# Optimization experiments

Measured on AMD Instinct MI355X. Metric: run time of the kernel, lower is better.

## Reference

```python
import jax, jax.numpy as jnp
import numpy as np

USER_NUM = 100000
ITEM_NUM = 50000
EMBED = 64
N_LAYERS = 3
E_RATE = 2000000
E_TRUST = 500000
E_PRED = 100000


def setup_inputs() -> dict:
    key = jax.random.key(0)
    ks = jax.random.split(key, 10)
    return {
        "emb_user": jax.random.normal(ks[0], (USER_NUM, EMBED), dtype=jnp.float32),
        "emb_item": jax.random.normal(ks[1], (ITEM_NUM, EMBED), dtype=jnp.float32),
        "rate_u": jax.random.randint(ks[2], (E_RATE,), 0, USER_NUM, dtype=jnp.int32),
        "rate_i": jax.random.randint(ks[3], (E_RATE,), 0, ITEM_NUM, dtype=jnp.int32),
        "trust_src": jax.random.randint(ks[4], (E_TRUST,), 0, USER_NUM, dtype=jnp.int32),
        "trust_dst": jax.random.randint(ks[5], (E_TRUST,), 0, USER_NUM, dtype=jnp.int32),
        "pos_u": jax.random.randint(ks[6], (E_PRED,), 0, USER_NUM, dtype=jnp.int32),
        "pos_i": jax.random.randint(ks[7], (E_PRED,), 0, ITEM_NUM, dtype=jnp.int32),
        "neg_u": jax.random.randint(ks[8], (E_PRED,), 0, USER_NUM, dtype=jnp.int32),
        "neg_i": jax.random.randint(ks[9], (E_PRED,), 0, ITEM_NUM, dtype=jnp.int32),
    }


def _degrees(idx, n):
    # float degree counts, clamped to >=1 (DGL GraphConv clamps zero degrees)
    d = jax.ops.segment_sum(jnp.ones_like(idx, dtype=jnp.float32), idx, num_segments=n)
    return jnp.maximum(d, 1.0)


def _gcn_conv(h_src, src, dst, n_dst, deg_src, deg_dst):
    # GraphConv(norm='both', weight=False, bias=False):
    # out[v] = deg(v)^-1/2 * sum_{u->v} deg(u)^-1/2 * h[u]
    ns = jax.lax.rsqrt(deg_src)
    nd = jax.lax.rsqrt(deg_dst)
    msg = (h_src * ns[:, None])[src]          # [E, D] gather
    agg = jax.ops.segment_sum(msg, dst, num_segments=n_dst)
    return agg * nd[:, None]


def reference(emb_user, emb_item, rate_u, rate_i, trust_src, trust_dst,
              pos_u, pos_i, neg_u, neg_i):
    nU, nI = emb_user.shape[0], emb_item.shape[0]
    deg_u = _degrees(rate_u, nU)       # user degree in rate graph (out for rate, in for rated-by)
    deg_i = _degrees(rate_i, nI)       # item degree in rate graph
    deg_ts = _degrees(trust_src, nU)
    deg_td = _degrees(trust_dst, nU)

    res_u, res_i = emb_user, emb_item
    cur_u, cur_i = emb_user, emb_item
    for _ in range(N_LAYERS):
        # item -> user ('rated-by'): src deg = deg_i, dst deg = deg_u
        new_u = _gcn_conv(cur_i, rate_i, rate_u, nU, deg_i, deg_u)
        # user -> item ('rate')
        new_i = _gcn_conv(cur_u, rate_u, rate_i, nI, deg_u, deg_i)
        # user -> user ('trust'), added into user output
        new_u = new_u + _gcn_conv(cur_u, trust_src, trust_dst, nU, deg_ts, deg_td)
        res_u = res_u + new_u
        res_i = res_i + new_i
        cur_u, cur_i = new_u, new_i

    scale = 1.0 / (N_LAYERS + 1)
    res_u = res_u * scale
    res_i = res_i * scale

    # HeteroDotProductPredictor on 'rate' etype: u_dot_v -> [E, 1]
    pos_score = jnp.sum(res_u[pos_u] * res_i[pos_i], axis=-1, keepdims=True)
    neg_score = jnp.sum(res_u[neg_u] * res_i[neg_i], axis=-1, keepdims=True)
    return pos_score, neg_score
```

## Files before the change

kernel.cpp:

```cpp
#include <hip/hip_runtime.h>
#include <hip/hip_fp16.h>

#define NU 100000
#define NI 50000
#define D  64
#define CAPU 64
#define CAPI 96
#define CAPT 32
#define BS 256

#define NB1 256
#define KPB1 391
#define CAPB1 9216
#define NB2 256
#define KPB2 196
#define CAPB2 9216
#define NB3 128
#define KPB3 782
#define CAPB3 4864
#define NB4 128
#define CAPB4 4864
#define GR 224
#define GT 32

typedef unsigned long long u64;

__global__ void __launch_bounds__(1024) k_binAll(
    const int* __restrict__ ru, const int* __restrict__ ri,
    const int* __restrict__ ts, const int* __restrict__ td,
    int* __restrict__ bc1, int* __restrict__ bc2,
    int* __restrict__ bc3, int* __restrict__ bc4,
    u64* __restrict__ bins1, u64* __restrict__ bins2,
    u64* __restrict__ bins3, u64* __restrict__ bins4,
    int E_rate, int E_trust)
{
    __shared__ int cnt[512];
    __shared__ int base[512];
    int b = blockIdx.x, tid = threadIdx.x;
    if (b < GR) {
        if (tid < 512) cnt[tid] = 0;
        __syncthreads();
        for (int c0 = b * 1024; c0 < E_rate; c0 += GR * 1024) {
            int e = c0 + tid;
            if (e < E_rate) {
                int u = ru[e], it = ri[e];
                atomicAdd(&cnt[u / KPB1], 1);
                atomicAdd(&cnt[256 + it / KPB2], 1);
            }
        }
        __syncthreads();
        if (tid < 256)      base[tid] = atomicAdd(&bc1[tid], cnt[tid]);
        else if (tid < 512) base[tid] = atomicAdd(&bc2[tid - 256], cnt[tid]);
        __syncthreads();
        if (tid < 512) cnt[tid] = 0;
        __syncthreads();
        for (int c0 = b * 1024; c0 < E_rate; c0 += GR * 1024) {
            int e = c0 + tid;
            if (e < E_rate) {
                int u = ru[e], it = ri[e];
                int b1 = u / KPB1, b2 = it / KPB2;
                int r1 = atomicAdd(&cnt[b1], 1);
                int o1 = base[b1] + r1;
                if (o1 < CAPB1) bins1[(size_t)b1 * CAPB1 + o1] = ((u64)u << 32) | (unsigned)it;
                int r2 = atomicAdd(&cnt[256 + b2], 1);
                int o2 = base[256 + b2] + r2;
                if (o2 < CAPB2) bins2[(size_t)b2 * CAPB2 + o2] = ((u64)it << 32) | (unsigned)u;
            }
        }
    } else {
        int bb = b - GR;
        if (tid < 256) cnt[tid] = 0;
        __syncthreads();
        for (int c0 = bb * 1024; c0 < E_trust; c0 += GT * 1024) {
            int e = c0 + tid;
            if (e < E_trust) {
                int s = ts[e], dd = td[e];
                atomicAdd(&cnt[dd / KPB3], 1);
                atomicAdd(&cnt[128 + s / KPB3], 1);
            }
        }
        __syncthreads();
        if (tid < 128)      base[tid] = atomicAdd(&bc3[tid], cnt[tid]);
        else if (tid < 256) base[tid] = atomicAdd(&bc4[tid - 128], cnt[tid]);
        __syncthreads();
        if (tid < 256) cnt[tid] = 0;
        __syncthreads();
        for (int c0 = bb * 1024; c0 < E_trust; c0 += GT * 1024) {
            int e = c0 + tid;
            if (e < E_trust) {
                int s = ts[e], dd = td[e];
                int b3 = dd / KPB3, b4 = s / KPB3;
                int r3 = atomicAdd(&cnt[b3], 1);
                int o3 = base[b3] + r3;
                if (o3 < CAPB3) bins3[(size_t)b3 * CAPB3 + o3] = ((u64)dd << 32) | (unsigned)s;
                int r4 = atomicAdd(&cnt[128 + b4], 1);
                int o4 = base[128 + b4] + r4;
                if (o4 < CAPB4) bins4[(size_t)b4 * CAPB4 + o4] = ((u64)s << 32);
            }
        }
    }
}

__global__ void __launch_bounds__(512) k_buildAll(
    const u64* __restrict__ bins1, const u64* __restrict__ bins2,
    const u64* __restrict__ bins3, const u64* __restrict__ bins4,
    const int* __restrict__ bc1, const int* __restrict__ bc2,
    const int* __restrict__ bc3, const int* __restrict__ bc4,
    int* __restrict__ colU, int* __restrict__ colI, int* __restrict__ colT,
    int* __restrict__ degU, int* __restrict__ degI,
    int* __restrict__ degT, int* __restrict__ degS)
{
    __shared__ int cnt[KPB3];
    int b = blockIdx.x, tid = threadIdx.x;
    const u64* bins; int n, k0, kpb, colcap, nmax; int* col; int* deg;
    if (b < NB1) {
        bins = bins1 + (size_t)b * CAPB1; n = bc1[b]; if (n > CAPB1) n = CAPB1;
        k0 = b * KPB1; kpb = KPB1; colcap = CAPU; col = colU; deg = degU; nmax = NU;
    } else if (b < NB1 + NB2) {
        int q = b - NB1;
        bins = bins2 + (size_t)q * CAPB2; n = bc2[q]; if (n > CAPB2) n = CAPB2;
        k0 = q * KPB2; kpb = KPB2; colcap = CAPI; col = colI; deg = degI; nmax = NI;
    } else if (b < NB1 + NB2 + NB3) {
        int q = b - NB1 - NB2;
        bins = bins3 + (size_t)q * CAPB3; n = bc3[q]; if (n > CAPB3) n = CAPB3;
        k0 = q * KPB3; kpb = KPB3; colcap = CAPT; col = colT; deg = degT; nmax = NU;
    } else {
        int q = b - NB1 - NB2 - NB3;
        bins = bins4 + (size_t)q * CAPB4; n = bc4[q]; if (n > CAPB4) n = CAPB4;
        k0 = q * KPB3; kpb = KPB3; colcap = 0; col = nullptr; deg = degS; nmax = NU;
    }
    for (int t = tid; t < kpb; t += 512) cnt[t] = 0;
    __syncthreads();
    if (col) {
        for (int i = tid; i < n; i += 512) {
            u64 e = bins[i];
            int k = (int)(e >> 32);
            int v = (int)(e & 0xffffffffu);
            int c = atomicAdd(&cnt[k - k0], 1);
            if (c < colcap) col[(size_t)k * colcap + c] = v;
        }
    } else {
        for (int i = tid; i < n; i += 512) {
            int k = (int)(bins[i] >> 32);
            atomicAdd(&cnt[k - k0], 1);
        }
    }
    __syncthreads();
    for (int t = tid; t < kpb; t += 512) {
        int k = k0 + t;
        if (k < nmax) {
            int c = cnt[t];
            if (colcap && c > colcap) c = colcap;
            deg[k] = c;
        }
    }
}

__global__ void k_degrs(const int* __restrict__ degU, const int* __restrict__ degI,
                        const int* __restrict__ degT, const int* __restrict__ degS,
                        float* __restrict__ rs_u, float* __restrict__ rs_i,
                        float* __restrict__ rs_td, float* __restrict__ rs_ts) {
    int i = blockIdx.x * blockDim.x + threadIdx.x;
    if (i < NU) {
        int a = degU[i]; rs_u[i]  = rsqrtf((float)(a < 1 ? 1 : a));
        int b = degT[i]; rs_td[i] = rsqrtf((float)(b < 1 ? 1 : b));
        int c = degS[i]; rs_ts[i] = rsqrtf((float)(c < 1 ? 1 : c));
    }
    if (i < NI) {
        int a = degI[i]; rs_i[i] = rsqrtf((float)(a < 1 ? 1 : a));
    }
}

__global__ void k_inith(const float* __restrict__ src, uint2* __restrict__ cur,
                        uint2* __restrict__ res, int n4) {
    int i = blockIdx.x * blockDim.x + threadIdx.x;
    if (i >= n4) return;
    float4 v = ((const float4*)src)[i];
    uint2 u;
    u.x = ((unsigned)__half_as_ushort(__float2half(v.y)) << 16) |
           (unsigned)__half_as_ushort(__float2half(v.x));
    u.y = ((unsigned)__half_as_ushort(__float2half(v.w)) << 16) |
           (unsigned)__half_as_ushort(__float2half(v.z));
    cur[i] = u;
    res[i] = u;
}


__device__ __forceinline__ void gather32(const int* __restrict__ col, int b, int d,
                                         const float* __restrict__ rs,
                                         const __half2* __restrict__ rows, int gl,
                                         float2& acc) {
    int e = b + d;
    for (int k0 = b; k0 < e; k0 += 32) {
        int idx = k0 + gl;
        int   n = idx < e ? col[idx] : 0;
        float r = idx < e ? rs[n] : 0.f;
        #pragma unroll
        for (int j = 0; j < 32; ++j) {
            int   nn = __shfl(n, j, 32);
            float rr = __shfl(r, j, 32);
            float2 f = __half22float2(rows[(size_t)nn * 32 + gl]);
            acc.x += rr * f.x;
            acc.y += rr * f.y;
        }
    }
}

__device__ __forceinline__ void gather8(const int* __restrict__ col, int b, int d,
                                        const float* __restrict__ rs,
                                        const __half2* __restrict__ rows, int gl,
                                        float2& acc) {
    int e = b + d;
    int sub = gl & 7;
    for (int k0 = b; k0 < e; k0 += 8) {
        int idx = k0 + sub;
        int   n = idx < e ? col[idx] : 0;
        float r = idx < e ? rs[n] : 0.f;
        #pragma unroll
        for (int j = 0; j < 8; ++j) {
            int   nn = __shfl(n, j, 32);
            float rr = __shfl(r, j, 32);
            float2 f = __half22float2(rows[(size_t)nn * 32 + gl]);
            acc.x += rr * f.x;
            acc.y += rr * f.y;
        }
    }
}

__global__ void k_layer(const int* __restrict__ colU, const int* __restrict__ degU,
                        const int* __restrict__ colT, const int* __restrict__ degT,
                        const int* __restrict__ colI, const int* __restrict__ degI,
                        const float* __restrict__ rs_u, const float* __restrict__ rs_i,
                        const float* __restrict__ rs_ts, const float* __restrict__ rs_td,
                        const __half2* __restrict__ cu, const __half2* __restrict__ ci,
                        __half2* __restrict__ nu, __half2* __restrict__ ni,
                        __half2* __restrict__ resu, __half2* __restrict__ resi) {
    int b = blockIdx.x;
    int m = b % 3;
    int base = b / 3;
    int wid = threadIdx.x >> 6;
    int lane = threadIdx.x & 63;
    int grp = lane >> 5;
    int gl  = lane & 31;
    if (m < 2) {
        int node = ((base * 2 + m) * 4 + wid) * 2 + grp;
        if (node >= NU) return;
        float2 acc = {0.f, 0.f}, acc2 = {0.f, 0.f};
        gather32(colU, node * CAPU, degU[node], rs_i, ci, gl, acc);
        gather8 (colT, node * CAPT, degT[node], rs_ts, cu, gl, acc2);
        float su = rs_u[node], st = rs_td[node];
        float vx = su * acc.x + st * acc2.x;
        float vy = su * acc.y + st * acc2.y;
        size_t o = (size_t)node * 32 + gl;
        nu[o] = __floats2half2_rn(vx, vy);
        float2 old = __half22float2(resu[o]);
        resu[o] = __floats2half2_rn(old.x + vx, old.y + vy);
    } else {
        int node = (base * 4 + wid) * 2 + grp;
        if (node >= NI) return;
        float2 acc = {0.f, 0.f};
        gather32(colI, node * CAPI, degI[node], rs_u, cu, gl, acc);
        float si = rs_i[node];
        float vx = si * acc.x, vy = si * acc.y;
        size_t o = (size_t)node * 32 + gl;
        ni[o] = __floats2half2_rn(vx, vy);
        float2 old = __half22float2(resi[o]);
        resi[o] = __floats2half2_rn(old.x + vx, old.y + vy);
    }
}


__global__ void k_pred(const int* __restrict__ pu, const int* __restrict__ pi,
                       const int* __restrict__ nuv, const int* __restrict__ niv,
                       const __half2* __restrict__ ru, const __half2* __restrict__ ri,
                       float* __restrict__ out, int E) {
    long long tid = (long long)blockIdx.x * blockDim.x + threadIdx.x;
    int e = (int)(tid >> 4);
    int c2 = ((int)tid & 15) * 2;
    if (e >= 2 * E) return;
    int ee = (e < E) ? e : e - E;
    int u  = (e < E) ? pu[ee] : nuv[ee];
    int it = (e < E) ? pi[ee] : niv[ee];
    float2 a0 = __half22float2(ru[(size_t)u  * 32 + c2]);
    float2 a1 = __half22float2(ru[(size_t)u  * 32 + c2 + 1]);
    float2 b0 = __half22float2(ri[(size_t)it * 32 + c2]);
    float2 b1 = __half22float2(ri[(size_t)it * 32 + c2 + 1]);
    float s = a0.x * b0.x + a0.y * b0.y + a1.x * b1.x + a1.y * b1.y;
    s += __shfl_xor(s, 1); s += __shfl_xor(s, 2);
    s += __shfl_xor(s, 4); s += __shfl_xor(s, 8);
    if (((int)tid & 15) == 0) out[e] = s * (1.0f / 16.0f);
}

extern "C" void kernel_launch(void* const* d_in, const int* in_sizes, int n_in,
                              void* d_out, int out_size, void* d_ws, size_t ws_size,
                              hipStream_t stream) {
    const float* emb_u  = (const float*)d_in[0];
    const float* emb_i  = (const float*)d_in[1];
    const int* rate_u   = (const int*)d_in[2];
    const int* rate_i   = (const int*)d_in[3];
    const int* trust_s  = (const int*)d_in[4];
    const int* trust_d  = (const int*)d_in[5];
    const int* pos_u    = (const int*)d_in[6];
    const int* pos_i    = (const int*)d_in[7];
    const int* neg_u    = (const int*)d_in[8];
    const int* neg_i    = (const int*)d_in[9];
    const int E_rate  = in_sizes[2];
    const int E_trust = in_sizes[4];
    const int E_pred  = in_sizes[6];

    int* iw   = (int*)d_ws;
    int* degU = iw;
    int* degI = degU + NU;
    int* degT = degI + NI;
    int* degS = degT + NU;
    int* bc1  = degS + NU;
    int* bc2  = bc1 + NB1;
    int* bc3  = bc2 + NB2;
    int* bc4  = bc3 + NB3;
    int* colU = bc4 + NB4;
    int* colI = colU + (size_t)NU * CAPU;
    int* colT = colI + (size_t)NI * CAPI;
    float* rs_u  = (float*)(colT + (size_t)NU * CAPT);
    float* rs_i  = rs_u  + NU;
    float* rs_ts = rs_i  + NI;
    float* rs_td = rs_ts + NU;
    __half2* uA   = (__half2*)(rs_td + NU);
    __half2* uB   = uA + (size_t)NU * 32;
    __half2* iA   = uB + (size_t)NU * 32;
    __half2* iB   = iA + (size_t)NI * 32;
    __half2* res_u = iB + (size_t)NI * 32;
    __half2* res_i = res_u + (size_t)NU * 32;
    u64* bins1 = (u64*)uA;
    u64* bins2 = bins1 + (size_t)NB1 * CAPB1;
    u64* bins3 = bins2 + (size_t)NB2 * CAPB2;
    u64* bins4 = bins3 + (size_t)NB3 * CAPB3;

    hipMemsetAsync(bc1, 0, (NB1 + NB2 + NB3 + NB4) * sizeof(int), stream);

    k_binAll<<<GR + GT, 1024, 0, stream>>>(rate_u, rate_i, trust_s, trust_d,
                                           bc1, bc2, bc3, bc4,
                                           bins1, bins2, bins3, bins4,
                                           E_rate, E_trust);
    k_buildAll<<<NB1 + NB2 + NB3 + NB4, 512, 0, stream>>>(
        bins1, bins2, bins3, bins4, bc1, bc2, bc3, bc4,
        colU, colI, colT, degU, degI, degT, degS);

    k_degrs<<<(NU + BS - 1) / BS, BS, 0, stream>>>(degU, degI, degT, degS,
                                                   rs_u, rs_i, rs_td, rs_ts);

    k_inith<<<(NU * D / 4 + BS - 1) / BS, BS, 0, stream>>>(emb_u, (uint2*)uA, (uint2*)res_u, NU * D / 4);
    k_inith<<<(NI * D / 4 + BS - 1) / BS, BS, 0, stream>>>(emb_i, (uint2*)iA, (uint2*)res_i, NI * D / 4);

    __half2* cu = uA; __half2* nu_ = uB;
    __half2* ci = iA; __half2* ni_ = iB;
    for (int l = 0; l < 3; ++l) {
        k_layer<<<18750, BS, 0, stream>>>(colU, degU, colT, degT, colI, degI,
                                          rs_u, rs_i, rs_ts, rs_td,
                                          cu, ci, nu_, ni_, res_u, res_i);
        __half2* t;
        t = cu; cu = nu_; nu_ = t;
        t = ci; ci = ni_; ni_ = t;
    }

    long long tp = (long long)2 * E_pred * 16;
    k_pred<<<(unsigned)((tp + BS - 1) / BS), BS, 0, stream>>>(
        pos_u, pos_i, neg_u, neg_i, res_u, res_i, (float*)d_out, E_pred);
}
```

Before: 404.3 us.

## Partition neighbor lists by source-index range and split layer into user/item kernels

Adjacency lists are split by neighbor-index range: each node's list is filled from both ends, in two halves for users and trust and four quarters for items. Each segment is then gathered separately, so neighbors of similar index are processed together, aiming for better cache locality on the embedding gathers. The fused layer kernel is also split into separate user and item kernels, which adds a launch per layer and a dependency between them. Degrees are packed as per-class counts and summed in k_degrs, and the extra gather calls add loop overhead for partially filled segments.

```diff
diff --git a/kernel.cpp b/kernel.cpp
--- a/kernel.cpp
+++ b/kernel.cpp
@@ -110,48 +110,106 @@
     int* __restrict__ degU, int* __restrict__ degI,
     int* __restrict__ degT, int* __restrict__ degS)
 {
-    __shared__ int cnt[KPB3];
+    __shared__ int cnt[1568];
     int b = blockIdx.x, tid = threadIdx.x;
-    const u64* bins; int n, k0, kpb, colcap, nmax; int* col; int* deg;
     if (b < NB1) {
-        bins = bins1 + (size_t)b * CAPB1; n = bc1[b]; if (n > CAPB1) n = CAPB1;
-        k0 = b * KPB1; kpb = KPB1; colcap = CAPU; col = colU; deg = degU; nmax = NU;
+        const u64* bins = bins1 + (size_t)b * CAPB1;
+        int n = bc1[b]; if (n > CAPB1) n = CAPB1;
+        int k0 = b * KPB1;
+        for (int t = tid; t < 2 * KPB1; t += 512) cnt[t] = 0;
+        __syncthreads();
+        for (int i = tid; i < n; i += 512) {
+            u64 e = bins[i];
+            int k = (int)(e >> 32) - k0;
+            int v = (int)(e & 0xffffffffu);
+            int cls = v >= (NI / 2);
+            int c = atomicAdd(&cnt[k + cls * KPB1], 1);
+            if (c < CAPU) {
+                int slot = cls ? (CAPU - 1 - c) : c;
+                colU[(size_t)(k0 + k) * CAPU + slot] = v;
+            }
+        }
+        __syncthreads();
+        for (int t = tid; t < KPB1; t += 512) {
+            int k = k0 + t;
+            if (k < NU) {
+                int c0 = cnt[t];          if (c0 > CAPU) c0 = CAPU;
+                int c1 = cnt[t + KPB1];   if (c1 > CAPU) c1 = CAPU;
+                degU[k] = c0 | (c1 << 16);
+            }
+        }
     } else if (b < NB1 + NB2) {
         int q = b - NB1;
-        bins = bins2 + (size_t)q * CAPB2; n = bc2[q]; if (n > CAPB2) n = CAPB2;
-        k0 = q * KPB2; kpb = KPB2; colcap = CAPI; col = colI; deg = degI; nmax = NI;
+        const u64* bins = bins2 + (size_t)q * CAPB2;
+        int n = bc2[q]; if (n > CAPB2) n = CAPB2;
+        int k0 = q * KPB2;
+        for (int t = tid; t < 4 * KPB2; t += 512) cnt[t] = 0;
+        __syncthreads();
+        for (int i = tid; i < n; i += 512) {
+            u64 e = bins[i];
+            int k = (int)(e >> 32) - k0;
+            int v = (int)(e & 0xffffffffu);
+            int cls = v / (NU / 4);
+            int c = atomicAdd(&cnt[k + cls * KPB2], 1);
+            if (c < 48) {
+                int slot = (cls == 0) ? c : (cls == 1) ? (47 - c)
+                         : (cls == 2) ? (48 + c) : (95 - c);
+                colI[(size_t)(k0 + k) * CAPI + slot] = v;
+            }
+        }
+        __syncthreads();
+        for (int t = tid; t < KPB2; t += 512) {
+            int k = k0 + t;
+            if (k < NI) {
+                int c0 = cnt[t];            if (c0 > 48) c0 = 48;
+                int c1 = cnt[t + KPB2];     if (c1 > 48) c1 = 48;
+                int c2 = cnt[t + 2 * KPB2]; if (c2 > 48) c2 = 48;
+                int c3 = cnt[t + 3 * KPB2]; if (c3 > 48) c3 = 48;
+                degI[k] = c0 | (c1 << 8) | (c2 << 16) | (c3 << 24);
+            }
+        }
     } else if (b < NB1 + NB2 + NB3) {
         int q = b - NB1 - NB2;
-        bins = bins3 + (size_t)q * CAPB3; n = bc3[q]; if (n > CAPB3) n = CAPB3;
-        k0 = q * KPB3; kpb = KPB3; colcap = CAPT; col = colT; deg = degT; nmax = NU;
+        const u64* bins = bins3 + (size_t)q * CAPB3;
+        int n = bc3[q]; if (n > CAPB3) n = CAPB3;
+        int k0 = q * KPB3;
+        for (int t = tid; t < 2 * KPB3; t += 512) cnt[t] = 0;
+        __syncthreads();
+        for (int i = tid; i < n; i += 512) {
+            u64 e = bins[i];
+            int k = (int)(e >> 32) - k0;
+            int v = (int)(e & 0xffffffffu);
+            int cls = v >= (NU / 2);
+            int c = atomicAdd(&cnt[k + cls * KPB3], 1);
+            if (c < CAPT) {
+                int slot = cls ? (CAPT - 1 - c) : c;
+                colT[(size_t)(k0 + k) * CAPT + slot] = v;
+            }
+        }
+        __syncthreads();
+        for (int t = tid; t < KPB3; t += 512) {
+            int k = k0 + t;
+            if (k < NU) {
+                int c0 = cnt[t];          if (c0 > CAPT) c0 = CAPT;
+                int c1 = cnt[t + KPB3];   if (c1 > CAPT) c1 = CAPT;
+                degT[k] = c0 | (c1 << 16);
+            }
+        }
     } else {
         int q = b - NB1 - NB2 - NB3;
-        bins = bins4 + (size_t)q * CAPB4; n = bc4[q]; if (n > CAPB4) n = CAPB4;
-        k0 = q * KPB3; kpb = KPB3; colcap = 0; col = nullptr; deg = degS; nmax = NU;
-    }
-    for (int t = tid; t < kpb; t += 512) cnt[t] = 0;
-    __syncthreads();
-    if (col) {
-        for (int i = tid; i < n; i += 512) {
-            u64 e = bins[i];
-            int k = (int)(e >> 32);
-            int v = (int)(e & 0xffffffffu);
-            int c = atomicAdd(&cnt[k - k0], 1);
-            if (c < colcap) col[(size_t)k * colcap + c] = v;
-        }
-    } else {
+        const u64* bins = bins4 + (size_t)q * CAPB4;
+        int n = bc4[q]; if (n > CAPB4) n = CAPB4;
+        int k0 = q * KPB3;
+        for (int t = tid; t < KPB3; t += 512) cnt[t] = 0;
+        __syncthreads();
         for (int i = tid; i < n; i += 512) {
             int k = (int)(bins[i] >> 32);
             atomicAdd(&cnt[k - k0], 1);
         }
-    }
-    __syncthreads();
-    for (int t = tid; t < kpb; t += 512) {
-        int k = k0 + t;
-        if (k < nmax) {
-            int c = cnt[t];
-            if (colcap && c > colcap) c = colcap;
-            deg[k] = c;
+        __syncthreads();
+        for (int t = tid; t < KPB3; t += 512) {
+            int k = k0 + t;
+            if (k < NU) degS[k] = cnt[t];
         }
     }
 }
@@ -162,12 +220,17 @@
                         float* __restrict__ rs_td, float* __restrict__ rs_ts) {
     int i = blockIdx.x * blockDim.x + threadIdx.x;
     if (i < NU) {
-        int a = degU[i]; rs_u[i]  = rsqrtf((float)(a < 1 ? 1 : a));
-        int b = degT[i]; rs_td[i] = rsqrtf((float)(b < 1 ? 1 : b));
-        int c = degS[i]; rs_ts[i] = rsqrtf((float)(c < 1 ? 1 : c));
+        int du = (degU[i] & 0xffff) + (degU[i] >> 16);
+        rs_u[i]  = rsqrtf((float)(du < 1 ? 1 : du));
+        int dt = (degT[i] & 0xffff) + (degT[i] >> 16);
+        rs_td[i] = rsqrtf((float)(dt < 1 ? 1 : dt));
+        int ds = degS[i];
+        rs_ts[i] = rsqrtf((float)(ds < 1 ? 1 : ds));
     }
     if (i < NI) {
-        int a = degI[i]; rs_i[i] = rsqrtf((float)(a < 1 ? 1 : a));
+        int d = degI[i];
+        int di = (d & 255) + ((d >> 8) & 255) + ((d >> 16) & 255) + ((d >> 24) & 255);
+        rs_i[i] = rsqrtf((float)(di < 1 ? 1 : di));
     }
 }
 
@@ -227,46 +290,62 @@
     }
 }
 
-__global__ void k_layer(const int* __restrict__ colU, const int* __restrict__ degU,
-                        const int* __restrict__ colT, const int* __restrict__ degT,
-                        const int* __restrict__ colI, const int* __restrict__ degI,
-                        const float* __restrict__ rs_u, const float* __restrict__ rs_i,
-                        const float* __restrict__ rs_ts, const float* __restrict__ rs_td,
-                        const __half2* __restrict__ cu, const __half2* __restrict__ ci,
-                        __half2* __restrict__ nu, __half2* __restrict__ ni,
-                        __half2* __restrict__ resu, __half2* __restrict__ resi) {
-    int b = blockIdx.x;
-    int m = b % 3;
-    int base = b / 3;
+__global__ void k_user(const int* __restrict__ colU, const int* __restrict__ degU,
+                       const int* __restrict__ colT, const int* __restrict__ degT,
+                       const float* __restrict__ rs_u, const float* __restrict__ rs_i,
+                       const float* __restrict__ rs_ts, const float* __restrict__ rs_td,
+                       const __half2* __restrict__ cu, const __half2* __restrict__ ci,
+                       __half2* __restrict__ nu, __half2* __restrict__ resu) {
     int wid = threadIdx.x >> 6;
     int lane = threadIdx.x & 63;
     int grp = lane >> 5;
     int gl  = lane & 31;
-    if (m < 2) {
-        int node = ((base * 2 + m) * 4 + wid) * 2 + grp;
-        if (node >= NU) return;
-        float2 acc = {0.f, 0.f}, acc2 = {0.f, 0.f};
-        gather32(colU, node * CAPU, degU[node], rs_i, ci, gl, acc);
-        gather8 (colT, node * CAPT, degT[node], rs_ts, cu, gl, acc2);
-        float su = rs_u[node], st = rs_td[node];
-        float vx = su * acc.x + st * acc2.x;
-        float vy = su * acc.y + st * acc2.y;
-        size_t o = (size_t)node * 32 + gl;
-        nu[o] = __floats2half2_rn(vx, vy);
-        float2 old = __half22float2(resu[o]);
-        resu[o] = __floats2half2_rn(old.x + vx, old.y + vy);
-    } else {
-        int node = (base * 4 + wid) * 2 + grp;
-        if (node >= NI) return;
-        float2 acc = {0.f, 0.f};
-        gather32(colI, node * CAPI, degI[node], rs_u, cu, gl, acc);
-        float si = rs_i[node];
-        float vx = si * acc.x, vy = si * acc.y;
-        size_t o = (size_t)node * 32 + gl;
-        ni[o] = __floats2half2_rn(vx, vy);
-        float2 old = __half22float2(resi[o]);
-        resi[o] = __floats2half2_rn(old.x + vx, old.y + vy);
-    }
+    int node = (blockIdx.x * 4 + wid) * 2 + grp;
+    if (node >= NU) return;
+    int d = degU[node];
+    int l0 = d & 0xffff, l1 = d >> 16;
+    int base = node * CAPU;
+    float2 acc = {0.f, 0.f}, acc2 = {0.f, 0.f};
+    gather32(colU, base, l0, rs_i, ci, gl, acc);
+    gather32(colU, base + CAPU - l1, l1, rs_i, ci, gl, acc);
+    int dT = degT[node];
+    int t0 = dT & 0xffff, t1 = dT >> 16;
+    int baseT = node * CAPT;
+    gather8(colT, baseT, t0, rs_ts, cu, gl, acc2);
+    gather8(colT, baseT + CAPT - t1, t1, rs_ts, cu, gl, acc2);
+    float su = rs_u[node], st = rs_td[node];
+    float vx = su * acc.x + st * acc2.x;
+    float vy = su * acc.y + st * acc2.y;
+    size_t o = (size_t)node * 32 + gl;
+    nu[o] = __floats2half2_rn(vx, vy);
+    float2 old = __half22float2(resu[o]);
+    resu[o] = __floats2half2_rn(old.x + vx, old.y + vy);
+}
+
+__global__ void k_item(const int* __restrict__ colI, const int* __restrict__ degI,
+                       const float* __restrict__ rs_i, const float* __restrict__ rs_u,
+                       const __half2* __restrict__ cu,
+                       __half2* __restrict__ ni, __half2* __restrict__ resi) {
+    int wid = threadIdx.x >> 6;
+    int lane = threadIdx.x & 63;
+    int grp = lane >> 5;
+    int gl  = lane & 31;
+    int node = (blockIdx.x * 4 + wid) * 2 + grp;
+    if (node >= NI) return;
+    int d = degI[node];
+    int b0 = d & 255, b1 = (d >> 8) & 255, b2 = (d >> 16) & 255, b3 = (d >> 24) & 255;
+    int base = node * CAPI;
+    float2 acc = {0.f, 0.f};
+    gather32(colI, base,            b0, rs_u, cu, gl, acc);
+    gather32(colI, base + 48 - b1,  b1, rs_u, cu, gl, acc);
+    gather32(colI, base + 48,       b2, rs_u, cu, gl, acc);
+    gather32(colI, base + CAPI - b3, b3, rs_u, cu, gl, acc);
+    float si = rs_i[node];
+    float vx = si * acc.x, vy = si * acc.y;
+    size_t o = (size_t)node * 32 + gl;
+    ni[o] = __floats2half2_rn(vx, vy);
+    float2 old = __half22float2(resi[o]);
+    resi[o] = __floats2half2_rn(old.x + vx, old.y + vy);
 }
 
 
@@ -354,9 +433,11 @@
     __half2* cu = uA; __half2* nu_ = uB;
     __half2* ci = iA; __half2* ni_ = iB;
     for (int l = 0; l < 3; ++l) {
-        k_layer<<<18750, BS, 0, stream>>>(colU, degU, colT, degT, colI, degI,
-                                          rs_u, rs_i, rs_ts, rs_td,
-                                          cu, ci, nu_, ni_, res_u, res_i);
+        k_user<<<12500, BS, 0, stream>>>(colU, degU, colT, degT,
+                                         rs_u, rs_i, rs_ts, rs_td,
+                                         cu, ci, nu_, res_u);
+        k_item<<<6250, BS, 0, stream>>>(colI, degI, rs_i, rs_u,
+                                        cu, ni_, res_i);
         __half2* t;
         t = cu; cu = nu_; nu_ = t;
         t = ci; ci = ni_; ni_ = t;
```

Result: slower. 610.6 us (+51.0%).

## Pre-scale stored embeddings by source norm and use 16-lane row gathers

Applied to the files above, without the earlier changes.

Embeddings are now stored already multiplied by their source-degree rsqrt, so the rate-graph gathers skip the per-neighbor rs load and multiply. The trust-graph weight is folded into a single rs_ts/rs_u factor. Each row is handled by 16 lanes loading 8-byte uint2 values instead of 32 lanes loading 4 bytes, which packs four nodes per wavefront and halves the grid. A zero sentinel row replaces the masked rs lookup for padding. Storing pre-scaled values in fp16 shifts where rounding happens and may change precision slightly.

```diff
diff --git a/kernel.cpp b/kernel.cpp
--- a/kernel.cpp
+++ b/kernel.cpp
@@ -159,116 +159,142 @@
 __global__ void k_degrs(const int* __restrict__ degU, const int* __restrict__ degI,
                         const int* __restrict__ degT, const int* __restrict__ degS,
                         float* __restrict__ rs_u, float* __restrict__ rs_i,
-                        float* __restrict__ rs_td, float* __restrict__ rs_ts) {
+                        float* __restrict__ rs_td, float* __restrict__ rs_tsu) {
     int i = blockIdx.x * blockDim.x + threadIdx.x;
     if (i < NU) {
-        int a = degU[i]; rs_u[i]  = rsqrtf((float)(a < 1 ? 1 : a));
+        int a = degU[i]; float ru = rsqrtf((float)(a < 1 ? 1 : a));
+        rs_u[i] = ru;
         int b = degT[i]; rs_td[i] = rsqrtf((float)(b < 1 ? 1 : b));
-        int c = degS[i]; rs_ts[i] = rsqrtf((float)(c < 1 ? 1 : c));
+        int c = degS[i]; rs_tsu[i] = rsqrtf((float)(c < 1 ? 1 : c)) / ru;
     }
     if (i < NI) {
         int a = degI[i]; rs_i[i] = rsqrtf((float)(a < 1 ? 1 : a));
     }
 }
 
-__global__ void k_inith(const float* __restrict__ src, uint2* __restrict__ cur,
-                        uint2* __restrict__ res, int n4) {
+__device__ __forceinline__ uint2 pack4(float a, float b, float c, float d) {
+    __half2 lo = __floats2half2_rn(a, b);
+    __half2 hi = __floats2half2_rn(c, d);
+    uint2 r;
+    r.x = *(unsigned*)&lo;
+    r.y = *(unsigned*)&hi;
+    return r;
+}
+
+__global__ void k_inith(const float* __restrict__ src, const float* __restrict__ rs,
+                        uint2* __restrict__ curS, uint2* __restrict__ res, int n16) {
     int i = blockIdx.x * blockDim.x + threadIdx.x;
-    if (i >= n4) return;
+    if (i >= n16) return;
     float4 v = ((const float4*)src)[i];
-    uint2 u;
-    u.x = ((unsigned)__half_as_ushort(__float2half(v.y)) << 16) |
-           (unsigned)__half_as_ushort(__float2half(v.x));
-    u.y = ((unsigned)__half_as_ushort(__float2half(v.w)) << 16) |
-           (unsigned)__half_as_ushort(__float2half(v.z));
-    cur[i] = u;
-    res[i] = u;
-}
-
-
-__device__ __forceinline__ void gather32(const int* __restrict__ col, int b, int d,
-                                         const float* __restrict__ rs,
-                                         const __half2* __restrict__ rows, int gl,
-                                         float2& acc) {
-    int e = b + d;
-    for (int k0 = b; k0 < e; k0 += 32) {
-        int idx = k0 + gl;
-        int   n = idx < e ? col[idx] : 0;
-        float r = idx < e ? rs[n] : 0.f;
-        #pragma unroll
-        for (int j = 0; j < 32; ++j) {
-            int   nn = __shfl(n, j, 32);
-            float rr = __shfl(r, j, 32);
-            float2 f = __half22float2(rows[(size_t)nn * 32 + gl]);
-            acc.x += rr * f.x;
-            acc.y += rr * f.y;
-        }
-    }
-}
-
-__device__ __forceinline__ void gather8(const int* __restrict__ col, int b, int d,
-                                        const float* __restrict__ rs,
-                                        const __half2* __restrict__ rows, int gl,
-                                        float2& acc) {
-    int e = b + d;
-    int sub = gl & 7;
-    for (int k0 = b; k0 < e; k0 += 8) {
-        int idx = k0 + sub;
-        int   n = idx < e ? col[idx] : 0;
-        float r = idx < e ? rs[n] : 0.f;
-        #pragma unroll
-        for (int j = 0; j < 8; ++j) {
-            int   nn = __shfl(n, j, 32);
-            float rr = __shfl(r, j, 32);
-            float2 f = __half22float2(rows[(size_t)nn * 32 + gl]);
-            acc.x += rr * f.x;
-            acc.y += rr * f.y;
-        }
-    }
+    float s = rs[i >> 4];
+    res[i]  = pack4(v.x, v.y, v.z, v.w);
+    curS[i] = pack4(s * v.x, s * v.y, s * v.z, s * v.w);
+}
+
+__global__ void k_zrow(uint2* uA, uint2* uB, uint2* iA, uint2* iB) {
+    int t = threadIdx.x;
+    int e = t & 15;
+    uint2 z; z.x = 0; z.y = 0;
+    if (t < 16)      uA[(size_t)NU * 16 + e] = z;
+    else if (t < 32) uB[(size_t)NU * 16 + e] = z;
+    else if (t < 48) iA[(size_t)NI * 16 + e] = z;
+    else             iB[(size_t)NI * 16 + e] = z;
 }
 
 __global__ void k_layer(const int* __restrict__ colU, const int* __restrict__ degU,
                         const int* __restrict__ colT, const int* __restrict__ degT,
                         const int* __restrict__ colI, const int* __restrict__ degI,
                         const float* __restrict__ rs_u, const float* __restrict__ rs_i,
-                        const float* __restrict__ rs_ts, const float* __restrict__ rs_td,
-                        const __half2* __restrict__ cu, const __half2* __restrict__ ci,
-                        __half2* __restrict__ nu, __half2* __restrict__ ni,
-                        __half2* __restrict__ resu, __half2* __restrict__ resi) {
+                        const float* __restrict__ rs_td, const float* __restrict__ rs_tsu,
+                        const uint2* __restrict__ cuR, const uint2* __restrict__ ciS,
+                        uint2* __restrict__ nuR, uint2* __restrict__ niS,
+                        uint2* __restrict__ resu, uint2* __restrict__ resi) {
     int b = blockIdx.x;
     int m = b % 3;
     int base = b / 3;
     int wid = threadIdx.x >> 6;
     int lane = threadIdx.x & 63;
-    int grp = lane >> 5;
-    int gl  = lane & 31;
+    int grp = lane >> 4;
+    int gl  = lane & 15;
     if (m < 2) {
-        int node = ((base * 2 + m) * 4 + wid) * 2 + grp;
+        int node = ((base * 2 + m) * 4 + wid) * 4 + grp;
         if (node >= NU) return;
-        float2 acc = {0.f, 0.f}, acc2 = {0.f, 0.f};
-        gather32(colU, node * CAPU, degU[node], rs_i, ci, gl, acc);
-        gather8 (colT, node * CAPT, degT[node], rs_ts, cu, gl, acc2);
+        float4 acc = {0.f, 0.f, 0.f, 0.f};
+        {
+            int bb = node * CAPU, e = bb + degU[node];
+            for (int k0 = bb; k0 < e; k0 += 16) {
+                int idx = k0 + gl;
+                int n = idx < e ? colU[idx] : NI;
+                #pragma unroll
+                for (int j = 0; j < 16; ++j) {
+                    int nn = __shfl(n, j, 16);
+                    uint2 q = ciS[(size_t)nn * 16 + gl];
+                    float2 f = __half22float2(*(__half2*)&q.x);
+                    float2 g = __half22float2(*(__half2*)&q.y);
+                    acc.x += f.x; acc.y += f.y; acc.z += g.x; acc.w += g.y;
+                }
+            }
+        }
+        float4 acc2 = {0.f, 0.f, 0.f, 0.f};
+        {
+            int bb = node * CAPT, e = bb + degT[node];
+            int sub = gl & 7;
+            for (int k0 = bb; k0 < e; k0 += 8) {
+                int idx = k0 + sub;
+                int n = idx < e ? colT[idx] : NU;
+                float w = idx < e ? rs_tsu[n] : 0.f;
+                #pragma unroll
+                for (int j = 0; j < 8; ++j) {
+                    int nn  = __shfl(n, j, 16);
+                    float ww = __shfl(w, j, 16);
+                    uint2 q = cuR[(size_t)nn * 16 + gl];
+                    float2 f = __half22float2(*(__half2*)&q.x);
+                    float2 g = __half22float2(*(__half2*)&q.y);
+                    acc2.x += ww * f.x; acc2.y += ww * f.y;
+                    acc2.z += ww * g.x; acc2.w += ww * g.y;
+                }
+            }
+        }
         float su = rs_u[node], st = rs_td[node];
         float vx = su * acc.x + st * acc2.x;
         float vy = su * acc.y + st * acc2.y;
-        size_t o = (size_t)node * 32 + gl;
-        nu[o] = __floats2half2_rn(vx, vy);
-        float2 old = __half22float2(resu[o]);
-        resu[o] = __floats2half2_rn(old.x + vx, old.y + vy);
+        float vz = su * acc.z + st * acc2.z;
+        float vw = su * acc.w + st * acc2.w;
+        size_t o = (size_t)node * 16 + gl;
+        nuR[o] = pack4(su * vx, su * vy, su * vz, su * vw);
+        uint2 r = resu[o];
+        float2 ra = __half22float2(*(__half2*)&r.x);
+        float2 rb = __half22float2(*(__half2*)&r.y);
+        resu[o] = pack4(ra.x + vx, ra.y + vy, rb.x + vz, rb.y + vw);
     } else {
-        int node = (base * 4 + wid) * 2 + grp;
+        int node = (base * 4 + wid) * 4 + grp;
         if (node >= NI) return;
-        float2 acc = {0.f, 0.f};
-        gather32(colI, node * CAPI, degI[node], rs_u, cu, gl, acc);
+        float4 acc = {0.f, 0.f, 0.f, 0.f};
+        {
+            int bb = node * CAPI, e = bb + degI[node];
+            for (int k0 = bb; k0 < e; k0 += 16) {
+                int idx = k0 + gl;
+                int n = idx < e ? colI[idx] : NU;
+                #pragma unroll
+                for (int j = 0; j < 16; ++j) {
+                    int nn = __shfl(n, j, 16);
+                    uint2 q = cuR[(size_t)nn * 16 + gl];
+                    float2 f = __half22float2(*(__half2*)&q.x);
+                    float2 g = __half22float2(*(__half2*)&q.y);
+                    acc.x += f.x; acc.y += f.y; acc.z += g.x; acc.w += g.y;
+                }
+            }
+        }
         float si = rs_i[node];
-        float vx = si * acc.x, vy = si * acc.y;
-        size_t o = (size_t)node * 32 + gl;
-        ni[o] = __floats2half2_rn(vx, vy);
-        float2 old = __half22float2(resi[o]);
-        resi[o] = __floats2half2_rn(old.x + vx, old.y + vy);
-    }
-}
-
+        float vx = si * acc.x, vy = si * acc.y, vz = si * acc.z, vw = si * acc.w;
+        size_t o = (size_t)node * 16 + gl;
+        niS[o] = pack4(si * vx, si * vy, si * vz, si * vw);
+        uint2 r = resi[o];
+        float2 ra = __half22float2(*(__half2*)&r.x);
+        float2 rb = __half22float2(*(__half2*)&r.y);
+        resi[o] = pack4(ra.x + vx, ra.y + vy, rb.x + vz, rb.y + vw);
+    }
+}
 
 __global__ void k_pred(const int* __restrict__ pu, const int* __restrict__ pi,
                        const int* __restrict__ nuv, const int* __restrict__ niv,
@@ -320,17 +346,17 @@
     int* colU = bc4 + NB4;
     int* colI = colU + (size_t)NU * CAPU;
     int* colT = colI + (size_t)NI * CAPI;
-    float* rs_u  = (float*)(colT + (size_t)NU * CAPT);
-    float* rs_i  = rs_u  + NU;
-    float* rs_ts = rs_i  + NI;
-    float* rs_td = rs_ts + NU;
-    __half2* uA   = (__half2*)(rs_td + NU);
-    __half2* uB   = uA + (size_t)NU * 32;
-    __half2* iA   = uB + (size_t)NU * 32;
-    __half2* iB   = iA + (size_t)NI * 32;
-    __half2* res_u = iB + (size_t)NI * 32;
-    __half2* res_i = res_u + (size_t)NU * 32;
-    u64* bins1 = (u64*)uA;
+    float* rs_u   = (float*)(colT + (size_t)NU * CAPT);
+    float* rs_i   = rs_u  + NU;
+    float* rs_td  = rs_i  + NI;
+    float* rs_tsu = rs_td + NU;
+    uint2* uRA  = (uint2*)(rs_tsu + NU);
+    uint2* uRB  = uRA + (size_t)(NU + 1) * 16;
+    uint2* iSA  = uRB + (size_t)(NU + 1) * 16;
+    uint2* iSB  = iSA + (size_t)(NI + 1) * 16;
+    uint2* res_u = iSB + (size_t)(NI + 1) * 16;
+    uint2* res_i = res_u + (size_t)NU * 16;
+    u64* bins1 = (u64*)uRA;
     u64* bins2 = bins1 + (size_t)NB1 * CAPB1;
     u64* bins3 = bins2 + (size_t)NB2 * CAPB2;
     u64* bins4 = bins3 + (size_t)NB3 * CAPB3;
@@ -346,23 +372,25 @@
         colU, colI, colT, degU, degI, degT, degS);
 
     k_degrs<<<(NU + BS - 1) / BS, BS, 0, stream>>>(degU, degI, degT, degS,
-                                                   rs_u, rs_i, rs_td, rs_ts);
-
-    k_inith<<<(NU * D / 4 + BS - 1) / BS, BS, 0, stream>>>(emb_u, (uint2*)uA, (uint2*)res_u, NU * D / 4);
-    k_inith<<<(NI * D / 4 + BS - 1) / BS, BS, 0, stream>>>(emb_i, (uint2*)iA, (uint2*)res_i, NI * D / 4);
-
-    __half2* cu = uA; __half2* nu_ = uB;
-    __half2* ci = iA; __half2* ni_ = iB;
+                                                   rs_u, rs_i, rs_td, rs_tsu);
+
+    k_inith<<<(NU * 16 + BS - 1) / BS, BS, 0, stream>>>(emb_u, rs_u, uRA, res_u, NU * 16);
+    k_inith<<<(NI * 16 + BS - 1) / BS, BS, 0, stream>>>(emb_i, rs_i, iSA, res_i, NI * 16);
+    k_zrow<<<1, 64, 0, stream>>>(uRA, uRB, iSA, iSB);
+
+    uint2* cu = uRA; uint2* nu_ = uRB;
+    uint2* ci = iSA; uint2* ni_ = iSB;
     for (int l = 0; l < 3; ++l) {
-        k_layer<<<18750, BS, 0, stream>>>(colU, degU, colT, degT, colI, degI,
-                                          rs_u, rs_i, rs_ts, rs_td,
-                                          cu, ci, nu_, ni_, res_u, res_i);
-        __half2* t;
+        k_layer<<<9375, BS, 0, stream>>>(colU, degU, colT, degT, colI, degI,
+                                         rs_u, rs_i, rs_td, rs_tsu,
+                                         cu, ci, nu_, ni_, res_u, res_i);
+        uint2* t;
         t = cu; cu = nu_; nu_ = t;
         t = ci; ci = ni_; ni_ = t;
     }
 
     long long tp = (long long)2 * E_pred * 16;
     k_pred<<<(unsigned)((tp + BS - 1) / BS), BS, 0, stream>>>(
-        pos_u, pos_i, neg_u, neg_i, res_u, res_i, (float*)d_out, E_pred);
-}
+        pos_u, pos_i, neg_u, neg_i, (const __half2*)res_u, (const __half2*)res_i,
+        (float*)d_out, E_pred);
+}
```

Result: faster. 366.3 us (-9.4%).
